# Performance work log

Hardware: AMD Instinct MI355X
Metric: run time of the kernel (lower is better)

The kernel has to match this reference:

```python
import jax, jax.numpy as jnp
import numpy as np

N_NODES = 25000
N_EDGES = 250000
F_IN = 32
F_OUT = 32
EDGE_DIM = 6
H1, H2 = 64, 128


def setup_inputs() -> dict:
    key = jax.random.key(0)
    ks = jax.random.split(key, 10)
    s = 0.05
    return {
        "x": jax.random.normal(ks[0], (N_NODES, F_IN), dtype=jnp.float32),
        "edge_attr": jax.random.normal(ks[1], (N_EDGES, EDGE_DIM), dtype=jnp.float32),
        # fnet MLP params: Linear(6->64), ReLU, Linear(64->128), ReLU, Linear(128->F_IN*F_OUT)
        "W1": jax.random.normal(ks[2], (H1, EDGE_DIM), dtype=jnp.float32) * s,
        "b1": jnp.zeros((H1,), dtype=jnp.float32),
        "W2": jax.random.normal(ks[3], (H2, H1), dtype=jnp.float32) * s,
        "b2": jnp.zeros((H2,), dtype=jnp.float32),
        "W3": jax.random.normal(ks[4], (F_IN * F_OUT, H2), dtype=jnp.float32) * s,
        "b3": jnp.zeros((F_IN * F_OUT,), dtype=jnp.float32),
        "edge_src": jax.random.randint(ks[5], (N_EDGES,), 0, N_NODES),
        "edge_dst": jax.random.randint(ks[6], (N_EDGES,), 0, N_NODES),
    }


def reference(x, edge_attr, W1, b1, W2, b2, W3, b3, edge_src, edge_dst):
    # fnet: per-edge MLP producing a dynamic filter theta_e of shape [F_OUT, F_IN]
    h = jax.nn.relu(edge_attr @ W1.T + b1)            # [E, H1]
    h = jax.nn.relu(h @ W2.T + b2)                    # [E, H2]
    theta = (h @ W3.T + b3).reshape(-1, F_OUT, F_IN)  # [E, F_OUT, F_IN]
    # gather source features, apply per-edge filter
    msg = jnp.einsum('eoi,ei->eo', theta, x[edge_src])  # [E, F_OUT]
    # scatter-mean over destination nodes (ECC averages over neighborhood)
    agg = jax.ops.segment_sum(msg, edge_dst, num_segments=N_NODES)
    deg = jax.ops.segment_sum(jnp.ones((msg.shape[0],), x.dtype), edge_dst,
                              num_segments=N_NODES)
    out = agg / jnp.maximum(deg, 1.0)[:, None]        # [N, F_OUT]
    return jax.nn.relu(out)                           # trailing 'r' in config
```

## Files before the change

### kernel.cpp

```cpp
#include <hip/hip_runtime.h>
#include <hip/hip_fp16.h>

#define N_NODES 25000
#define N_EDGES 250000
#define ED 6
#define H1 64
#define H2 128
#define NBLK 977
#define NCHUNK 33
#define CHUNK_USH 4096
#define W3S_USHORTS (NCHUNK*CHUNK_USH)
#define W2S_USHORTS (H2*H1)
#define SCAN_BLOCKS 98

typedef float f32x4 __attribute__((ext_vector_type(4)));
typedef _Float16 f16x8 __attribute__((ext_vector_type(8)));
typedef _Float16 f16x2 __attribute__((ext_vector_type(2)));
typedef __fp16 fp16x2 __attribute__((ext_vector_type(2)));
typedef unsigned int u32x4 __attribute__((ext_vector_type(4)));
typedef unsigned int u32x2 __attribute__((ext_vector_type(2)));

union F16x8U { u32x4 u; f16x8 h; };
union F16x2U { unsigned u; f16x2 h; };
union PKU    { fp16x2 p; unsigned u; };

__device__ __forceinline__ unsigned pkrtz(float lo, float hi) {
    PKU r; r.p = __builtin_amdgcn_cvt_pkrtz(lo, hi); return r.u;
}
__device__ __forceinline__ unsigned pk_mul_blo(unsigned h, unsigned x) {
    unsigned d;
    asm("v_pk_mul_f16 %0, %1, %2 op_sel:[0,0] op_sel_hi:[0,1]" : "=v"(d) : "v"(h), "v"(x));
    return d;
}
__device__ __forceinline__ unsigned pk_mul_bhi(unsigned h, unsigned x) {
    unsigned d;
    asm("v_pk_mul_f16 %0, %1, %2 op_sel:[1,0] op_sel_hi:[1,1]" : "=v"(d) : "v"(h), "v"(x));
    return d;
}
__device__ __forceinline__ f32x4 mfma16(f16x8 a, f16x8 b, f32x4 c) {
    return __builtin_amdgcn_mfma_f32_16x16x32_f16(a, b, c, 0, 0, 0);
}
__device__ __forceinline__ void gload16(const void* g, void* l) {
    __builtin_amdgcn_global_load_lds(
        (const __attribute__((address_space(1))) unsigned int*)g,
        (__attribute__((address_space(3))) unsigned int*)l, 16, 0, 0);
}

__global__ __launch_bounds__(256) void ecc_init(
    const float* __restrict__ W3, const float* __restrict__ b3,
    const float* __restrict__ W2,
    unsigned* __restrict__ cnt, unsigned short* __restrict__ w3s,
    unsigned short* __restrict__ w2s)
{
    int idx = blockIdx.x * 256 + threadIdx.x;
    if (idx < W3S_USHORTS) {
        int c = idx >> 12, r = idx & 4095;
        int p = r >> 7, kl = r & 127;
        int kp = c * 128 + kl;
        int o = ((p & 15) << 1) + (p >> 4);
        float v = 0.f;
        if (kp < 4096)      { int k = kp >> 5, i = kp & 31; v = W3[(o * 32 + i) * 128 + k]; }
        else if (kp < 4128) { v = b3[o * 32 + (kp - 4096)]; }
        int boff = ((p << 8) + (kl << 1)) ^ ((p & 7) << 4);
        __half hv = __float2half_rn(v);
        w3s[(c << 12) + (boff >> 1)] = *reinterpret_cast<unsigned short*>(&hv);
    }
    if (idx < W2S_USHORTS) {
        __half hv = __float2half_rn(W2[idx]);
        w2s[idx] = *reinterpret_cast<unsigned short*>(&hv);
    }
    if (idx < N_NODES) cnt[idx] = 0u;
}

__global__ __launch_bounds__(256) void ecc_hist(
    const int* __restrict__ dst, unsigned* __restrict__ cnt,
    unsigned* __restrict__ rank)
{
    int e = blockIdx.x * 256 + threadIdx.x;
    if (e < N_EDGES) rank[e] = atomicAdd(&cnt[dst[e]], 1u);
}

__global__ __launch_bounds__(256) void ecc_scan1(
    const unsigned* __restrict__ cnt, unsigned* __restrict__ off,
    unsigned* __restrict__ bsum)
{
    __shared__ unsigned s[256];
    const int t = threadIdx.x, i = blockIdx.x * 256 + t;
    unsigned v = (i < N_NODES) ? cnt[i] : 0u;
    s[t] = v; __syncthreads();
    #pragma unroll
    for (int d = 1; d < 256; d <<= 1) {
        unsigned add = (t >= d) ? s[t - d] : 0u;
        __syncthreads(); s[t] += add; __syncthreads();
    }
    if (i < N_NODES) off[i] = s[t] - v;
    if (t == 255) bsum[blockIdx.x] = s[255];
}

__global__ __launch_bounds__(128) void ecc_scan2(
    const unsigned* __restrict__ bsum, unsigned* __restrict__ bsumx)
{
    __shared__ unsigned s[128];
    const int t = threadIdx.x;
    unsigned v = (t < SCAN_BLOCKS) ? bsum[t] : 0u;
    s[t] = v; __syncthreads();
    #pragma unroll
    for (int d = 1; d < 128; d <<= 1) {
        unsigned add = (t >= d) ? s[t - d] : 0u;
        __syncthreads(); s[t] += add; __syncthreads();
    }
    if (t < SCAN_BLOCKS) bsumx[t] = s[t] - v;
}

__global__ __launch_bounds__(256) void ecc_scan3(
    unsigned* __restrict__ off, const unsigned* __restrict__ bsumx)
{
    int i = blockIdx.x * 256 + threadIdx.x;
    if (i < N_NODES) off[i] += bsumx[blockIdx.x];
    if (i == 0) off[N_NODES] = N_EDGES;
}

__global__ __launch_bounds__(256) void ecc_perm(
    const int* __restrict__ dst, const unsigned* __restrict__ off,
    const unsigned* __restrict__ rank, unsigned* __restrict__ perm)
{
    int e = blockIdx.x * 256 + threadIdx.x;
    if (e < N_EDGES) perm[off[dst[e]] + rank[e]] = (unsigned)e;
}

__global__ __launch_bounds__(256, 2) void ecc_fused(
    const float* __restrict__ x,   const float* __restrict__ ea,
    const float* __restrict__ W1,  const float* __restrict__ b1,
    const unsigned short* __restrict__ w2s, const float* __restrict__ b2,
    const unsigned short* __restrict__ w3s,
    const int* __restrict__ src,   const unsigned* __restrict__ perm,
    unsigned* __restrict__ msg32)
{
    __shared__ __align__(16) unsigned short sm[256 * H2];
    __shared__ __align__(16) unsigned short wbuf[2][CHUNK_USH];

    const int t = threadIdx.x;
    const int tile = blockIdx.x * 256;
    const int slot = tile + t;
    const bool ev = (slot < N_EDGES);
    const unsigned je = ev ? perm[slot] : 0u;

    const int w = t >> 6, l = t & 63, lr = l & 15, kg = l >> 4;

    gload16(w3s + t * 8,        &wbuf[0][t * 8]);
    gload16(w3s + 2048 + t * 8, &wbuf[0][2048 + t * 8]);

    {
        float a[ED];
        #pragma unroll
        for (int c = 0; c < ED; ++c) a[c] = ev ? ea[(long)je * ED + c] : 0.f;

        float h1[H1];
        #pragma unroll
        for (int o = 0; o < H1; ++o) {
            float acc = b1[o];
            #pragma unroll
            for (int c = 0; c < ED; ++c) acc = fmaf(W1[o * ED + c], a[c], acc);
            h1[o] = fmaxf(acc, 0.f);
        }
        #pragma unroll
        for (int q = 0; q < 8; ++q) {
            u32x4 pk;
            #pragma unroll
            for (int j = 0; j < 4; ++j)
                pk[j] = pkrtz(h1[q*8 + 2*j], h1[q*8 + 2*j + 1]);
            const int boff = (t * 128 + q * 16) ^ ((t & 7) << 4);
            *(u32x4*)((char*)sm + boff) = pk;
        }
    }

    unsigned xsh[4][4];
    #pragma unroll
    for (int mt = 0; mt < 4; ++mt) {
        const int er = tile + w * 64 + mt * 16 + lr;
        if (er < N_EDGES) {
            const float4* xp = (const float4*)(x + (long)src[perm[er]] * 32 + kg * 8);
            float4 v0 = xp[0], v1 = xp[1];
            xsh[mt][0] = pkrtz(v0.x, v0.y); xsh[mt][1] = pkrtz(v0.z, v0.w);
            xsh[mt][2] = pkrtz(v1.x, v1.y); xsh[mt][3] = pkrtz(v1.z, v1.w);
        } else {
            xsh[mt][0] = xsh[mt][1] = xsh[mt][2] = xsh[mt][3] = 0u;
        }
    }

    {
        F16x8U hb[4][2];
        #pragma unroll
        for (int ne = 0; ne < 4; ++ne) {
            const int er = w * 64 + ne * 16 + lr;
            #pragma unroll
            for (int ks = 0; ks < 2; ++ks) {
                const int boff = (er * 128 + ks * 64 + kg * 16) ^ ((er & 7) << 4);
                hb[ne][ks].u = *(const u32x4*)((const char*)sm + boff);
            }
        }
        __syncthreads();

        #pragma unroll
        for (int mo = 0; mo < 8; ++mo) {
            F16x8U a2[2];
            #pragma unroll
            for (int ks = 0; ks < 2; ++ks)
                a2[ks].u = *(const u32x4*)(w2s + (mo*16 + lr) * 64 + ks*32 + kg*8);
            const float4 bv = *(const float4*)(b2 + mo*16 + kg*4);
            #pragma unroll
            for (int ne = 0; ne < 4; ++ne) {
                f32x4 c = (f32x4){0.f, 0.f, 0.f, 0.f};
                c = mfma16(a2[0].h, hb[ne][0].h, c);
                c = mfma16(a2[1].h, hb[ne][1].h, c);
                const unsigned p0 = pkrtz(fmaxf(c[0]+bv.x, 0.f), fmaxf(c[1]+bv.y, 0.f));
                const unsigned p1 = pkrtz(fmaxf(c[2]+bv.z, 0.f), fmaxf(c[3]+bv.w, 0.f));
                const int er = w * 64 + ne * 16 + lr;
                const int boff = (er * 256 + (mo*16 + kg*4) * 2) ^ ((er & 7) << 4);
                *(u32x2*)((char*)sm + boff) = (u32x2){p0, p1};
            }
        }
    }

    f32x4 acc[4][2];
    #pragma unroll
    for (int mt = 0; mt < 4; ++mt)
        #pragma unroll
        for (int nt = 0; nt < 2; ++nt) acc[mt][nt] = (f32x4){0.f,0.f,0.f,0.f};

    const int swz = (lr & 7) << 4;
    __syncthreads();

    int cur = 0;
    #pragma unroll 1
    for (int c = 0; c < NCHUNK; ++c) {
        if (c + 1 < NCHUNK) {
            const unsigned short* gs = w3s + (c + 1) * CHUNK_USH + t * 8;
            gload16(gs,        &wbuf[cur ^ 1][t * 8]);
            gload16(gs + 2048, &wbuf[cur ^ 1][2048 + t * 8]);
        }
        const char* wb = (const char*)wbuf[cur];

        if (c < 32) {
            u32x2 hv[4];
            #pragma unroll
            for (int mt = 0; mt < 4; ++mt) {
                const int row = w * 64 + mt * 16 + lr;
                const int boff = (row * 256 + c * 8) ^ ((row & 7) << 4);
                hv[mt] = *(const u32x2*)((const char*)sm + boff);
            }
            #pragma unroll
            for (int kk = 0; kk < 4; ++kk) {
                const int akk = (lr * 256 + kg * 16 + kk * 64) ^ swz;
                F16x8U b0, b1;
                b0.u = *(const u32x4*)(wb + akk);
                b1.u = *(const u32x4*)(wb + akk + 4096);
                #pragma unroll
                for (int mt = 0; mt < 4; ++mt) {
                    const unsigned h01 = hv[mt][kk >> 1];
                    F16x8U af;
                    if (kk & 1) {
                        af.u[0] = pk_mul_bhi(h01, xsh[mt][0]);
                        af.u[1] = pk_mul_bhi(h01, xsh[mt][1]);
                        af.u[2] = pk_mul_bhi(h01, xsh[mt][2]);
                        af.u[3] = pk_mul_bhi(h01, xsh[mt][3]);
                    } else {
                        af.u[0] = pk_mul_blo(h01, xsh[mt][0]);
                        af.u[1] = pk_mul_blo(h01, xsh[mt][1]);
                        af.u[2] = pk_mul_blo(h01, xsh[mt][2]);
                        af.u[3] = pk_mul_blo(h01, xsh[mt][3]);
                    }
                    acc[mt][0] = mfma16(af.h, b0.h, acc[mt][0]);
                    acc[mt][1] = mfma16(af.h, b1.h, acc[mt][1]);
                }
            }
        } else {
            const int akk = (lr * 256 + kg * 16) ^ swz;
            F16x8U b0, b1;
            b0.u = *(const u32x4*)(wb + akk);
            b1.u = *(const u32x4*)(wb + akk + 4096);
            #pragma unroll
            for (int mt = 0; mt < 4; ++mt) {
                F16x8U af;
                af.u = (u32x4){xsh[mt][0], xsh[mt][1], xsh[mt][2], xsh[mt][3]};
                acc[mt][0] = mfma16(af.h, b0.h, acc[mt][0]);
                acc[mt][1] = mfma16(af.h, b1.h, acc[mt][1]);
            }
        }
        __syncthreads();
        cur ^= 1;
    }

    #pragma unroll
    for (int mt = 0; mt < 4; ++mt) {
        #pragma unroll
        for (int r = 0; r < 4; ++r) {
            const int j = tile + w * 64 + mt * 16 + kg * 4 + r;
            if (j < N_EDGES)
                msg32[(long)j * 16 + lr] = pkrtz(acc[mt][0][r], acc[mt][1][r]);
        }
    }
}

__global__ __launch_bounds__(256) void ecc_gather(
    const unsigned* __restrict__ msg32, const unsigned* __restrict__ off,
    float* __restrict__ out)
{
    const int t = threadIdx.x;
    const int q = t & 15;
    const int n = blockIdx.x * 16 + (t >> 4);
    if (n >= N_NODES) return;
    const unsigned lo = off[n], hi = off[n + 1];
    float s0 = 0.f, s1 = 0.f;
    for (unsigned j = lo; j < hi; ++j) {
        F16x2U v; v.u = msg32[(long)j * 16 + q];
        s0 += (float)v.h[0];
        s1 += (float)v.h[1];
    }
    const float dg = fmaxf((float)(hi - lo), 1.f);
    ((float2*)(out + (long)n * 32))[q] =
        make_float2(fmaxf(s0 / dg, 0.f), fmaxf(s1 / dg, 0.f));
}

extern "C" void kernel_launch(void* const* d_in, const int* in_sizes, int n_in,
                              void* d_out, int out_size, void* d_ws, size_t ws_size,
                              hipStream_t stream) {
    const float* x   = (const float*)d_in[0];
    const float* ea  = (const float*)d_in[1];
    const float* W1  = (const float*)d_in[2];
    const float* b1  = (const float*)d_in[3];
    const float* W2  = (const float*)d_in[4];
    const float* b2  = (const float*)d_in[5];
    const float* W3  = (const float*)d_in[6];
    const float* b3  = (const float*)d_in[7];
    const int*   src = (const int*)d_in[8];
    const int*   dst = (const int*)d_in[9];
    float* out = (float*)d_out;

    char* p = (char*)d_ws;
    unsigned short* w3s = (unsigned short*)p; p += W3S_USHORTS * 2;
    unsigned short* w2s = (unsigned short*)p; p += 16384;
    unsigned* cnt   = (unsigned*)p; p += 100096;
    unsigned* off   = (unsigned*)p; p += 100352;
    unsigned* bsum  = (unsigned*)p; p += 512;
    unsigned* bsumx = (unsigned*)p; p += 512;
    unsigned* rank  = (unsigned*)p; p += 1000192;
    unsigned* perm  = (unsigned*)p; p += 1000192;
    unsigned* msg32 = (unsigned*)p;

    ecc_init<<<(W3S_USHORTS + 255) / 256, 256, 0, stream>>>(W3, b3, W2, cnt, w3s, w2s);
    ecc_hist<<<NBLK, 256, 0, stream>>>(dst, cnt, rank);
    ecc_scan1<<<SCAN_BLOCKS, 256, 0, stream>>>(cnt, off, bsum);
    ecc_scan2<<<1, 128, 0, stream>>>(bsum, bsumx);
    ecc_scan3<<<SCAN_BLOCKS, 256, 0, stream>>>(off, bsumx);
    ecc_perm<<<NBLK, 256, 0, stream>>>(dst, off, rank, perm);
    ecc_fused<<<NBLK, 256, 0, stream>>>(x, ea, W1, b1, w2s, b2, w3s, src, perm, msg32);
    ecc_gather<<<(N_NODES + 15) / 16, 256, 0, stream>>>(msg32, off, out);
}
```

Measured before the change: 129.2 us.

## Stream W3 fragments directly from global into registers, drop LDS double buffer

The W3 filter weights are now stored row-contiguous (32 rows × 4224 halfs) and each lane loads its MFMA B fragments straight from global memory (L2-resident) into registers. A software double buffer with sched_barriers replaces the LDS staging. This removes the per-chunk __syncthreads and the LDS buffer traffic. In exchange it adds register pressure and global or L2 load latency that the register double buffer must hide.

```diff
diff --git a/kernel.cpp b/kernel.cpp
--- a/kernel.cpp
+++ b/kernel.cpp
@@ -7,11 +7,11 @@
 #define H1 64
 #define H2 128
 #define NBLK 977
-#define NCHUNK 33
-#define CHUNK_USH 4096
-#define W3S_USHORTS (NCHUNK*CHUNK_USH)
+#define K_TOT 4224
+#define W3S_USHORTS (32*K_TOT)
 #define W2S_USHORTS (H2*H1)
 #define SCAN_BLOCKS 98
+#define ROWB (K_TOT*2)
 
 typedef float f32x4 __attribute__((ext_vector_type(4)));
 typedef _Float16 f16x8 __attribute__((ext_vector_type(8)));
@@ -40,11 +40,6 @@
 __device__ __forceinline__ f32x4 mfma16(f16x8 a, f16x8 b, f32x4 c) {
     return __builtin_amdgcn_mfma_f32_16x16x32_f16(a, b, c, 0, 0, 0);
 }
-__device__ __forceinline__ void gload16(const void* g, void* l) {
-    __builtin_amdgcn_global_load_lds(
-        (const __attribute__((address_space(1))) unsigned int*)g,
-        (__attribute__((address_space(3))) unsigned int*)l, 16, 0, 0);
-}
 
 __global__ __launch_bounds__(256) void ecc_init(
     const float* __restrict__ W3, const float* __restrict__ b3,
@@ -54,16 +49,13 @@
 {
     int idx = blockIdx.x * 256 + threadIdx.x;
     if (idx < W3S_USHORTS) {
-        int c = idx >> 12, r = idx & 4095;
-        int p = r >> 7, kl = r & 127;
-        int kp = c * 128 + kl;
+        int p = idx / K_TOT, kp = idx % K_TOT;
         int o = ((p & 15) << 1) + (p >> 4);
         float v = 0.f;
         if (kp < 4096)      { int k = kp >> 5, i = kp & 31; v = W3[(o * 32 + i) * 128 + k]; }
         else if (kp < 4128) { v = b3[o * 32 + (kp - 4096)]; }
-        int boff = ((p << 8) + (kl << 1)) ^ ((p & 7) << 4);
         __half hv = __float2half_rn(v);
-        w3s[(c << 12) + (boff >> 1)] = *reinterpret_cast<unsigned short*>(&hv);
+        w3s[idx] = *reinterpret_cast<unsigned short*>(&hv);
     }
     if (idx < W2S_USHORTS) {
         __half hv = __float2half_rn(W2[idx]);
@@ -137,7 +129,6 @@
     unsigned* __restrict__ msg32)
 {
     __shared__ __align__(16) unsigned short sm[256 * H2];
-    __shared__ __align__(16) unsigned short wbuf[2][CHUNK_USH];
 
     const int t = threadIdx.x;
     const int tile = blockIdx.x * 256;
@@ -146,9 +137,6 @@
     const unsigned je = ev ? perm[slot] : 0u;
 
     const int w = t >> 6, l = t & 63, lr = l & 15, kg = l >> 4;
-
-    gload16(w3s + t * 8,        &wbuf[0][t * 8]);
-    gload16(w3s + 2048 + t * 8, &wbuf[0][2048 + t * 8]);
 
     {
         float a[ED];
@@ -187,6 +175,8 @@
             xsh[mt][0] = xsh[mt][1] = xsh[mt][2] = xsh[mt][3] = 0u;
         }
     }
+
+    __syncthreads();
 
     {
         F16x8U hb[4][2];
@@ -228,68 +218,76 @@
         #pragma unroll
         for (int nt = 0; nt < 2; ++nt) acc[mt][nt] = (f32x4){0.f,0.f,0.f,0.f};
 
-    const int swz = (lr & 7) << 4;
+    const char* gb0 = (const char*)w3s + lr * ROWB + kg * 16;
+    const char* gb1 = gb0 + 16 * ROWB;
+
     __syncthreads();
 
-    int cur = 0;
+    F16x8U BA0[4], BA1[4], BB0[4], BB1[4];
+
+#define LOADB(S0, S1, c) do {                                              \
+        const char* _p0 = gb0 + (c) * 256;                                 \
+        const char* _p1 = gb1 + (c) * 256;                                 \
+        S0[0].u = *(const u32x4*)(_p0);       S0[1].u = *(const u32x4*)(_p0 + 64);  \
+        S0[2].u = *(const u32x4*)(_p0 + 128); S0[3].u = *(const u32x4*)(_p0 + 192); \
+        S1[0].u = *(const u32x4*)(_p1);       S1[1].u = *(const u32x4*)(_p1 + 64);  \
+        S1[2].u = *(const u32x4*)(_p1 + 128); S1[3].u = *(const u32x4*)(_p1 + 192); \
+    } while (0)
+
+#define COMPUTE(S0, S1, c) do {                                            \
+        u32x2 hv[4];                                                       \
+        _Pragma("unroll")                                                  \
+        for (int mt = 0; mt < 4; ++mt) {                                   \
+            const int row = w * 64 + mt * 16 + lr;                         \
+            const int boff = (row * 256 + (c) * 8) ^ ((row & 7) << 4);     \
+            hv[mt] = *(const u32x2*)((const char*)sm + boff);              \
+        }                                                                  \
+        _Pragma("unroll")                                                  \
+        for (int kk = 0; kk < 4; ++kk) {                                   \
+            _Pragma("unroll")                                              \
+            for (int mt = 0; mt < 4; ++mt) {                               \
+                const unsigned h01 = hv[mt][kk >> 1];                      \
+                F16x8U af;                                                 \
+                if (kk & 1) {                                              \
+                    af.u[0] = pk_mul_bhi(h01, xsh[mt][0]);                 \
+                    af.u[1] = pk_mul_bhi(h01, xsh[mt][1]);                 \
+                    af.u[2] = pk_mul_bhi(h01, xsh[mt][2]);                 \
+                    af.u[3] = pk_mul_bhi(h01, xsh[mt][3]);                 \
+                } else {                                                   \
+                    af.u[0] = pk_mul_blo(h01, xsh[mt][0]);                 \
+                    af.u[1] = pk_mul_blo(h01, xsh[mt][1]);                 \
+                    af.u[2] = pk_mul_blo(h01, xsh[mt][2]);                 \
+                    af.u[3] = pk_mul_blo(h01, xsh[mt][3]);                 \
+                }                                                          \
+                acc[mt][0] = mfma16(af.h, S0[kk].h, acc[mt][0]);           \
+                acc[mt][1] = mfma16(af.h, S1[kk].h, acc[mt][1]);           \
+            }                                                              \
+        }                                                                  \
+    } while (0)
+
+    LOADB(BA0, BA1, 0);
     #pragma unroll 1
-    for (int c = 0; c < NCHUNK; ++c) {
-        if (c + 1 < NCHUNK) {
-            const unsigned short* gs = w3s + (c + 1) * CHUNK_USH + t * 8;
-            gload16(gs,        &wbuf[cur ^ 1][t * 8]);
-            gload16(gs + 2048, &wbuf[cur ^ 1][2048 + t * 8]);
-        }
-        const char* wb = (const char*)wbuf[cur];
-
-        if (c < 32) {
-            u32x2 hv[4];
-            #pragma unroll
-            for (int mt = 0; mt < 4; ++mt) {
-                const int row = w * 64 + mt * 16 + lr;
-                const int boff = (row * 256 + c * 8) ^ ((row & 7) << 4);
-                hv[mt] = *(const u32x2*)((const char*)sm + boff);
-            }
-            #pragma unroll
-            for (int kk = 0; kk < 4; ++kk) {
-                const int akk = (lr * 256 + kg * 16 + kk * 64) ^ swz;
-                F16x8U b0, b1;
-                b0.u = *(const u32x4*)(wb + akk);
-                b1.u = *(const u32x4*)(wb + akk + 4096);
-                #pragma unroll
-                for (int mt = 0; mt < 4; ++mt) {
-                    const unsigned h01 = hv[mt][kk >> 1];
-                    F16x8U af;
-                    if (kk & 1) {
-                        af.u[0] = pk_mul_bhi(h01, xsh[mt][0]);
-                        af.u[1] = pk_mul_bhi(h01, xsh[mt][1]);
-                        af.u[2] = pk_mul_bhi(h01, xsh[mt][2]);
-                        af.u[3] = pk_mul_bhi(h01, xsh[mt][3]);
-                    } else {
-                        af.u[0] = pk_mul_blo(h01, xsh[mt][0]);
-                        af.u[1] = pk_mul_blo(h01, xsh[mt][1]);
-                        af.u[2] = pk_mul_blo(h01, xsh[mt][2]);
-                        af.u[3] = pk_mul_blo(h01, xsh[mt][3]);
-                    }
-                    acc[mt][0] = mfma16(af.h, b0.h, acc[mt][0]);
-                    acc[mt][1] = mfma16(af.h, b1.h, acc[mt][1]);
-                }
-            }
-        } else {
-            const int akk = (lr * 256 + kg * 16) ^ swz;
-            F16x8U b0, b1;
-            b0.u = *(const u32x4*)(wb + akk);
-            b1.u = *(const u32x4*)(wb + akk + 4096);
-            #pragma unroll
-            for (int mt = 0; mt < 4; ++mt) {
-                F16x8U af;
-                af.u = (u32x4){xsh[mt][0], xsh[mt][1], xsh[mt][2], xsh[mt][3]};
-                acc[mt][0] = mfma16(af.h, b0.h, acc[mt][0]);
-                acc[mt][1] = mfma16(af.h, b1.h, acc[mt][1]);
-            }
-        }
-        __syncthreads();
-        cur ^= 1;
-    }
+    for (int c = 0; c < 32; c += 2) {
+        LOADB(BB0, BB1, c + 1);
+        __builtin_amdgcn_sched_barrier(0);
+        COMPUTE(BA0, BA1, c);
+        __builtin_amdgcn_sched_barrier(0);
+        LOADB(BA0, BA1, c + 2);
+        __builtin_amdgcn_sched_barrier(0);
+        COMPUTE(BB0, BB1, c + 1);
+        __builtin_amdgcn_sched_barrier(0);
+    }
+    {
+        #pragma unroll
+        for (int mt = 0; mt < 4; ++mt) {
+            F16x8U af;
+            af.u = (u32x4){xsh[mt][0], xsh[mt][1], xsh[mt][2], xsh[mt][3]};
+            acc[mt][0] = mfma16(af.h, BA0[0].h, acc[mt][0]);
+            acc[mt][1] = mfma16(af.h, BA1[0].h, acc[mt][1]);
+        }
+    }
+#undef LOADB
+#undef COMPUTE
 
     #pragma unroll
     for (int mt = 0; mt < 4; ++mt) {
```

Measured after the change: 188.6 us. 46.0% more time.
